# Kernel tuning notes

Measured on AMD Instinct MI355X. Metric: run time of the kernel, lower is better.

The kernel has to match this reference:

```python
import jax, jax.numpy as jnp
import numpy as np
import math

R1 = 1.0
R2 = 4.0
NBINS_XY = 4
NBINS_ZY = 4
PARTITIONS = NBINS_XY * NBINS_ZY * 2  # 32
TOPK = 200
TWO_PI = 2.0 * math.pi
PI = math.pi


def setup_inputs() -> dict:
    key = jax.random.key(0)
    k1, k2 = jax.random.split(key)
    # LiDAR-like coordinates, ~[-30, 30] meters
    sampled_vehicle_points = jax.random.normal(k1, (1024, 3), dtype=jnp.float32) * 20.0
    fusion_point = jax.random.normal(k2, (20000, 3), dtype=jnp.float32) * 20.0
    return {"sampled_vehicle_points": sampled_vehicle_points, "fusion_point": fusion_point}


def _compute_partitions_batch(q):
    # q: [S, K, 3]. rel[b, i, j] = q[b, j] - q[b, i]  (A.unsqueeze(1) - B.unsqueeze(2))
    rel = q[:, None, :, :] - q[:, :, None, :]  # [S, K, K, 3]
    angles_xy = jnp.fmod(jnp.arctan2(rel[..., 1], rel[..., 0]) + TWO_PI, TWO_PI)
    angles_zy = jnp.fmod(jnp.arctan2(rel[..., 1], rel[..., 2]) + TWO_PI, PI)
    xy_bins = jnp.floor(angles_xy / (TWO_PI / NBINS_XY))
    zy_bins = jnp.floor(angles_zy / (PI / NBINS_ZY))
    # hash(A, B, seed=NBINS_ZY): -1 where either < 0
    angle_ok = (xy_bins >= 0) & (zy_bins >= 0)
    angles_bins = jnp.where(angle_ok, xy_bins * NBINS_ZY + zy_bins, -1.0)
    D = jnp.sqrt(jnp.sum(rel * rel, axis=-1) + 1e-7)  # [S, K, K]
    dist_bins = jnp.where(D >= R2, 1.0, jnp.where(D >= R1, 0.0, -1.0))
    bin_ok = (dist_bins >= 0) & (angles_bins >= 0)
    bins = jnp.where(bin_ok, dist_bins * (NBINS_XY * NBINS_ZY) + angles_bins, -1.0)
    return bins  # [S, K, K] float, -1 for ignored


def reference(sampled_vehicle_points, fusion_point):
    # kNN query: K nearest fusion points for each sampled vehicle point
    d2 = jnp.sum(
        (sampled_vehicle_points[:, None, :] - fusion_point[None, :, :]) ** 2, axis=-1
    )  # [S, Nf]
    _, idx = jax.lax.top_k(-d2, TOPK)  # indices of TOPK smallest distances
    queried = fusion_point[idx]  # [S, K, 3]

    bins = _compute_partitions_batch(queried)  # [S, K, K]
    row0 = bins[:, 0, :]  # [S, K] — only row 0 is used by the loss
    # points_in_partition[s, p] = sum_j (row0[s, j] == p) + 1
    counts = jnp.sum(
        row0[:, :, None] == jnp.arange(PARTITIONS, dtype=bins.dtype)[None, None, :],
        axis=1,
    ).astype(jnp.float32) + 1.0  # [S, P]
    pip = counts / jnp.linalg.norm(counts, axis=-1, keepdims=True) * 4.0
    gt_dist = jax.nn.softmax(pip, axis=-1)
    return gt_dist
```

## Files before the change

kernel.cpp:

```cpp
#include <hip/hip_runtime.h>
#include <math.h>

#define KTOP 200
#define NPART 32
#define BLOCK 512
#define NHIST 2048
#define CAND_CAP 1024
#define WCAP 512
#define MAXIT 10

__device__ __forceinline__ float d2_ref(float ax, float ay, float az,
                                        float bx, float by, float bz) {
    float dx = __fsub_rn(ax, bx), dy = __fsub_rn(ay, by), dz = __fsub_rn(az, bz);
    return __fadd_rn(__fadd_rn(__fmul_rn(dx, dx), __fmul_rn(dy, dy)), __fmul_rn(dz, dz));
}

__device__ __forceinline__ unsigned key_of(const float* __restrict__ fus, int j,
                                           float vx, float vy, float vz) {
    return __float_as_uint(d2_ref(vx, vy, vz, fus[3*j], fus[3*j+1], fus[3*j+2]));
}

__device__ __forceinline__ int compute_bin(float rx, float ry, float rz) {
    const float TWO_PI_F = (float)6.283185307179586;
    const float PI_F     = (float)3.141592653589793;
    const float XY_W     = (float)(6.283185307179586 / 4.0);
    const float ZY_W     = (float)(3.141592653589793 / 4.0);

    float d2 = __fadd_rn(__fadd_rn(__fmul_rn(rx, rx), __fmul_rn(ry, ry)), __fmul_rn(rz, rz));
    float D  = sqrtf(__fadd_rn(d2, 1e-7f));
    float dist_bin;
    if (D >= 4.0f)      dist_bin = 1.0f;
    else if (D >= 1.0f) dist_bin = 0.0f;
    else                return -1;

    float axy = fmodf(atan2f(ry, rx) + TWO_PI_F, TWO_PI_F);
    float azy = fmodf(atan2f(ry, rz) + TWO_PI_F, PI_F);
    float xyb = floorf(__fdiv_rn(axy, XY_W));
    float zyb = floorf(__fdiv_rn(azy, ZY_W));
    if (!(xyb >= 0.0f && zyb >= 0.0f)) return -1;
    float ab  = xyb * 4.0f + zyb;
    int bin = (int)(dist_bin * 16.0f + ab);
    return bin;
}

__global__ __launch_bounds__(BLOCK, 4)
void shape_context_kernel(const float* __restrict__ veh,
                          const float* __restrict__ fus,
                          float* __restrict__ out,
                          int nfus) {
    const int b   = blockIdx.x;
    const int tid = threadIdx.x;
    const int lane = tid & 63;
    const int wid  = tid >> 6;

    __shared__ unsigned int hist[NHIST];
    __shared__ unsigned long long cand[CAND_CAP];
    __shared__ int wlist[WCAP];
    __shared__ unsigned int hist32[NPART];
    __shared__ unsigned int waveTot[BLOCK / 64];
    __shared__ unsigned int waveBase[BLOCK / 64];
    __shared__ unsigned int s_bucket, s_rem, s_bcount;
    __shared__ unsigned int s_minKey, s_minIdx;
    __shared__ int s_candCount, s_wcount;
    __shared__ float s_q0[3];
    __shared__ unsigned long long s_minPacked, s_lowBound;

    const float vx = veh[b * 3 + 0], vy = veh[b * 3 + 1], vz = veh[b * 3 + 2];
    const float4* fus4 = (const float4*)fus;
    const int ntrip = nfus >> 2;

    if (tid == 0) {
        s_minKey = 0xFFFFFFFFu; s_minIdx = 0xFFFFFFFFu;
        s_candCount = 0; s_wcount = 0;
    }
    for (int i = tid; i < NHIST; i += BLOCK) hist[i] = 0;
    if (tid < NPART) hist32[tid] = 0;
    __syncthreads();

    auto find_bucket = [&](unsigned remq) {
        const int PER = NHIST / BLOCK;
        int base = tid * PER;
        unsigned p = 0;
        #pragma unroll
        for (int i = 0; i < PER; i++) p += hist[base + i];
        unsigned incl = p;
        #pragma unroll
        for (int d = 1; d < 64; d <<= 1) {
            unsigned n = __shfl_up(incl, d, 64);
            if (lane >= d) incl += n;
        }
        if (lane == 63) waveTot[wid] = incl;
        __syncthreads();
        if (tid == 0) {
            unsigned acc = 0;
            for (int w = 0; w < BLOCK / 64; w++) { waveBase[w] = acc; acc += waveTot[w]; }
        }
        __syncthreads();
        unsigned excl = waveBase[wid] + incl - p;
        if (excl < remq && remq <= excl + p) {
            unsigned cum = excl;
            #pragma unroll
            for (int i = 0; i < PER; i++) {
                unsigned c = hist[base + i];
                if (cum + c >= remq) { s_bucket = base + i; s_rem = remq - cum; s_bcount = c; break; }
                cum += c;
            }
        }
        __syncthreads();
    };

    unsigned kreg[MAXIT][4];
    unsigned lmin = 0xFFFFFFFFu;
    #pragma unroll
    for (int it = 0; it < MAXIT; ++it) {
        int m = tid + it * BLOCK;
        if (m < ntrip) {
            float4 A = fus4[3 * m], Bq = fus4[3 * m + 1], Cq = fus4[3 * m + 2];
            float px0 = A.x,  py0 = A.y,  pz0 = A.z;
            float px1 = A.w,  py1 = Bq.x, pz1 = Bq.y;
            float px2 = Bq.z, py2 = Bq.w, pz2 = Cq.x;
            float px3 = Cq.y, py3 = Cq.z, pz3 = Cq.w;
            unsigned k0 = __float_as_uint(d2_ref(vx, vy, vz, px0, py0, pz0));
            unsigned k1 = __float_as_uint(d2_ref(vx, vy, vz, px1, py1, pz1));
            unsigned k2 = __float_as_uint(d2_ref(vx, vy, vz, px2, py2, pz2));
            unsigned k3 = __float_as_uint(d2_ref(vx, vy, vz, px3, py3, pz3));
            kreg[it][0] = k0; kreg[it][1] = k1; kreg[it][2] = k2; kreg[it][3] = k3;
            atomicAdd(&hist[k0 >> 21], 1u);
            atomicAdd(&hist[k1 >> 21], 1u);
            atomicAdd(&hist[k2 >> 21], 1u);
            atomicAdd(&hist[k3 >> 21], 1u);
            lmin = min(lmin, min(min(k0, k1), min(k2, k3)));
        } else {
            kreg[it][0] = kreg[it][1] = kreg[it][2] = kreg[it][3] = 0xFFFFFFFFu;
        }
    }
    for (int m = MAXIT * BLOCK + tid; m < ntrip; m += BLOCK) {
        #pragma unroll
        for (int q = 0; q < 4; ++q) {
            unsigned k = key_of(fus, 4 * m + q, vx, vy, vz);
            atomicAdd(&hist[k >> 21], 1u);
            lmin = min(lmin, k);
        }
    }
    for (int j = (nfus & ~3) + tid; j < nfus; j += BLOCK) {
        unsigned k = key_of(fus, j, vx, vy, vz);
        atomicAdd(&hist[k >> 21], 1u);
        lmin = min(lmin, k);
    }
    #pragma unroll
    for (int d = 32; d > 0; d >>= 1) lmin = min(lmin, __shfl_xor(lmin, d, 64));
    if (lane == 0) atomicMin(&s_minKey, lmin);
    __syncthreads();

    const unsigned mk = s_minKey;
    #pragma unroll
    for (int it = 0; it < MAXIT; ++it) {
        int m = tid + it * BLOCK;
        if (m < ntrip) {
            #pragma unroll
            for (int q = 0; q < 4; ++q)
                if (kreg[it][q] == mk) atomicMin(&s_minIdx, (unsigned)(4 * m + q));
        }
    }
    for (int m = MAXIT * BLOCK + tid; m < ntrip; m += BLOCK)
        #pragma unroll
        for (int q = 0; q < 4; ++q)
            if (key_of(fus, 4 * m + q, vx, vy, vz) == mk) atomicMin(&s_minIdx, (unsigned)(4 * m + q));
    for (int j = (nfus & ~3) + tid; j < nfus; j += BLOCK)
        if (key_of(fus, j, vx, vy, vz) == mk) atomicMin(&s_minIdx, (unsigned)j);

    find_bucket(KTOP);
    unsigned T = s_bucket;
    unsigned rem = s_rem;
    unsigned bcount = s_bcount;
    int shift = 21;

    if (tid == 0) {
        int idx0 = (int)s_minIdx;
        s_q0[0] = fus[idx0 * 3]; s_q0[1] = fus[idx0 * 3 + 1]; s_q0[2] = fus[idx0 * 3 + 2];
    }
    __syncthreads();
    const float q0x = s_q0[0], q0y = s_q0[1], q0z = s_q0[2];

    while (bcount > CAND_CAP && shift > 0) {
        int newshift = (shift > 11) ? (shift - 11) : 0;
        unsigned digmask = (1u << (shift - newshift)) - 1;
        for (int i = tid; i < NHIST; i += BLOCK) hist[i] = 0;
        __syncthreads();
        #pragma unroll
        for (int it = 0; it < MAXIT; ++it) {
            int m = tid + it * BLOCK;
            if (m < ntrip) {
                #pragma unroll
                for (int q = 0; q < 4; ++q) {
                    unsigned k = kreg[it][q];
                    if ((k >> shift) == T) atomicAdd(&hist[(k >> newshift) & digmask], 1u);
                }
            }
        }
        for (int m = MAXIT * BLOCK + tid; m < ntrip; m += BLOCK)
            #pragma unroll
            for (int q = 0; q < 4; ++q) {
                unsigned k = key_of(fus, 4 * m + q, vx, vy, vz);
                if ((k >> shift) == T) atomicAdd(&hist[(k >> newshift) & digmask], 1u);
            }
        for (int j = (nfus & ~3) + tid; j < nfus; j += BLOCK) {
            unsigned k = key_of(fus, j, vx, vy, vz);
            if ((k >> shift) == T) atomicAdd(&hist[(k >> newshift) & digmask], 1u);
        }
        __syncthreads();
        find_bucket(rem);
        T = (T << (shift - newshift)) | s_bucket;
        rem = s_rem;
        bcount = s_bcount;
        shift = newshift;
    }

    #pragma unroll
    for (int it = 0; it < MAXIT; ++it) {
        int m = tid + it * BLOCK;
        if (m < ntrip) {
            #pragma unroll
            for (int q = 0; q < 4; ++q) {
                unsigned k = kreg[it][q];
                unsigned hi = k >> shift;
                if (hi < T) {
                    int pos = atomicAdd(&s_wcount, 1);
                    if (pos < WCAP) wlist[pos] = 4 * m + q;
                } else if (hi == T) {
                    int pos = atomicAdd(&s_candCount, 1);
                    if (pos < CAND_CAP) cand[pos] = ((unsigned long long)k << 32) | (unsigned)(4 * m + q);
                }
            }
        }
    }
    for (int m = MAXIT * BLOCK + tid; m < ntrip; m += BLOCK)
        #pragma unroll
        for (int q = 0; q < 4; ++q) {
            unsigned k = key_of(fus, 4 * m + q, vx, vy, vz);
            unsigned hi = k >> shift;
            if (hi < T) { int pos = atomicAdd(&s_wcount, 1); if (pos < WCAP) wlist[pos] = 4 * m + q; }
            else if (hi == T) { int pos = atomicAdd(&s_candCount, 1); if (pos < CAND_CAP) cand[pos] = ((unsigned long long)k << 32) | (unsigned)(4 * m + q); }
        }
    for (int j = (nfus & ~3) + tid; j < nfus; j += BLOCK) {
        unsigned k = key_of(fus, j, vx, vy, vz);
        unsigned hi = k >> shift;
        if (hi < T) { int pos = atomicAdd(&s_wcount, 1); if (pos < WCAP) wlist[pos] = j; }
        else if (hi == T) { int pos = atomicAdd(&s_candCount, 1); if (pos < CAND_CAP) cand[pos] = ((unsigned long long)k << 32) | (unsigned)j; }
    }
    __syncthreads();

    const int cnt = s_candCount;
    if (cnt <= CAND_CAP) {
        for (int i = tid; i < cnt; i += BLOCK) {
            unsigned long long me = cand[i];
            int rank = 0;
            for (int k2 = 0; k2 < cnt; k2++) rank += (cand[k2] < me) ? 1 : 0;
            if (rank < (int)rem) {
                int pos = atomicAdd(&s_wcount, 1);
                if (pos < WCAP) wlist[pos] = (int)(me & 0xFFFFFFFFull);
            }
        }
    }
    __syncthreads();

    {
        int wc = s_wcount; if (wc > WCAP) wc = WCAP;
        for (int i = tid; i < wc; i += BLOCK) {
            int j = wlist[i];
            float fx = fus[3 * j], fy = fus[3 * j + 1], fz = fus[3 * j + 2];
            int bin = compute_bin(__fsub_rn(fx, q0x), __fsub_rn(fy, q0y), __fsub_rn(fz, q0z));
            if (bin >= 0 && bin < NPART) atomicAdd(&hist32[bin], 1u);
        }
    }
    __syncthreads();

    if (cnt > CAND_CAP) {
        if (tid == 0) s_lowBound = 0;
        __syncthreads();
        for (unsigned itx = 0; itx < rem; ++itx) {
            if (tid == 0) s_minPacked = ~0ull;
            __syncthreads();
            unsigned long long lowB = s_lowBound;
            unsigned long long lm = ~0ull;
            for (int j = tid; j < nfus; j += BLOCK) {
                unsigned k = key_of(fus, j, vx, vy, vz);
                if ((k >> shift) == T) {
                    unsigned long long p = ((unsigned long long)k << 32) | (unsigned)j;
                    if (p >= lowB && p < lm) lm = p;
                }
            }
            #pragma unroll
            for (int d = 32; d > 0; d >>= 1) {
                unsigned long long o = __shfl_xor(lm, d, 64);
                lm = (o < lm) ? o : lm;
            }
            if (lane == 0) atomicMin(&s_minPacked, lm);
            __syncthreads();
            if (tid == 0) {
                int jm = (int)(s_minPacked & 0xFFFFFFFFull);
                float fx = fus[jm * 3], fy = fus[jm * 3 + 1], fz = fus[jm * 3 + 2];
                int bin = compute_bin(__fsub_rn(fx, q0x), __fsub_rn(fy, q0y), __fsub_rn(fz, q0z));
                if (bin >= 0 && bin < NPART) hist32[bin] += 1u;
                s_lowBound = s_minPacked + 1;
            }
            __syncthreads();
        }
    }

    if (tid < NPART) {
        float c = (float)hist32[tid] + 1.0f;
        float ss = __fmul_rn(c, c);
        #pragma unroll
        for (int d = 16; d > 0; d >>= 1) ss += __shfl_xor(ss, d, 64);
        float v = __fmul_rn(__fdiv_rn(c, sqrtf(ss)), 4.0f);
        float mx = v;
        #pragma unroll
        for (int d = 16; d > 0; d >>= 1) mx = fmaxf(mx, __shfl_xor(mx, d, 64));
        float e = expf(v - mx);
        float sum = e;
        #pragma unroll
        for (int d = 16; d > 0; d >>= 1) sum += __shfl_xor(sum, d, 64);
        out[b * NPART + tid] = __fdiv_rn(e, sum);
    }
}

extern "C" void kernel_launch(void* const* d_in, const int* in_sizes, int n_in,
                              void* d_out, int out_size, void* d_ws, size_t ws_size,
                              hipStream_t stream) {
    const float* veh = (const float*)d_in[0];
    const float* fus = (const float*)d_in[1];
    float* out = (float*)d_out;
    int nveh = in_sizes[0] / 3;
    int nfus = in_sizes[1] / 3;
    shape_context_kernel<<<nveh, BLOCK, 0, stream>>>(veh, fus, out, nfus);
}
```

Before: 89.20 us.

## Pack top-bucket digits into registers and fuse min-key/index search

Per-thread key storage changes from forty 32-bit full keys to ten 64-bit words holding four 16-bit top digits each, and launch bounds are raised to allow 8 blocks per CU. The separate pass that finds the nearest point's index is replaced by a 64-bit packed (key,index) min reduction in the first pass. Refinement passes and candidate keys now recompute distances from global memory instead of reading cached keys, and the shared candidate buffer is halved to reduce LDS use. This trades extra recomputation and global loads for lower register and LDS pressure, aiming at higher occupancy.

```diff
diff --git a/kernel.cpp b/kernel.cpp
--- a/kernel.cpp
+++ b/kernel.cpp
@@ -5,7 +5,7 @@
 #define NPART 32
 #define BLOCK 512
 #define NHIST 2048
-#define CAND_CAP 1024
+#define CAND_CAP 512
 #define WCAP 512
 #define MAXIT 10
 
@@ -43,7 +43,7 @@
     return bin;
 }
 
-__global__ __launch_bounds__(BLOCK, 4)
+__global__ __launch_bounds__(BLOCK, 8)
 void shape_context_kernel(const float* __restrict__ veh,
                           const float* __restrict__ fus,
                           float* __restrict__ out,
@@ -60,7 +60,6 @@
     __shared__ unsigned int waveTot[BLOCK / 64];
     __shared__ unsigned int waveBase[BLOCK / 64];
     __shared__ unsigned int s_bucket, s_rem, s_bcount;
-    __shared__ unsigned int s_minKey, s_minIdx;
     __shared__ int s_candCount, s_wcount;
     __shared__ float s_q0[3];
     __shared__ unsigned long long s_minPacked, s_lowBound;
@@ -69,10 +68,7 @@
     const float4* fus4 = (const float4*)fus;
     const int ntrip = nfus >> 2;
 
-    if (tid == 0) {
-        s_minKey = 0xFFFFFFFFu; s_minIdx = 0xFFFFFFFFu;
-        s_candCount = 0; s_wcount = 0;
-    }
+    if (tid == 0) { s_minPacked = ~0ull; s_candCount = 0; s_wcount = 0; }
     for (int i = tid; i < NHIST; i += BLOCK) hist[i] = 0;
     if (tid < NPART) hist32[tid] = 0;
     __syncthreads();
@@ -109,29 +105,34 @@
         __syncthreads();
     };
 
-    unsigned kreg[MAXIT][4];
-    unsigned lmin = 0xFFFFFFFFu;
+    unsigned long long khi[MAXIT];
+    unsigned long long lmin = ~0ull;
     #pragma unroll
     for (int it = 0; it < MAXIT; ++it) {
         int m = tid + it * BLOCK;
         if (m < ntrip) {
             float4 A = fus4[3 * m], Bq = fus4[3 * m + 1], Cq = fus4[3 * m + 2];
-            float px0 = A.x,  py0 = A.y,  pz0 = A.z;
-            float px1 = A.w,  py1 = Bq.x, pz1 = Bq.y;
-            float px2 = Bq.z, py2 = Bq.w, pz2 = Cq.x;
-            float px3 = Cq.y, py3 = Cq.z, pz3 = Cq.w;
-            unsigned k0 = __float_as_uint(d2_ref(vx, vy, vz, px0, py0, pz0));
-            unsigned k1 = __float_as_uint(d2_ref(vx, vy, vz, px1, py1, pz1));
-            unsigned k2 = __float_as_uint(d2_ref(vx, vy, vz, px2, py2, pz2));
-            unsigned k3 = __float_as_uint(d2_ref(vx, vy, vz, px3, py3, pz3));
-            kreg[it][0] = k0; kreg[it][1] = k1; kreg[it][2] = k2; kreg[it][3] = k3;
+            unsigned k0 = __float_as_uint(d2_ref(vx, vy, vz, A.x,  A.y,  A.z));
+            unsigned k1 = __float_as_uint(d2_ref(vx, vy, vz, A.w,  Bq.x, Bq.y));
+            unsigned k2 = __float_as_uint(d2_ref(vx, vy, vz, Bq.z, Bq.w, Cq.x));
+            unsigned k3 = __float_as_uint(d2_ref(vx, vy, vz, Cq.y, Cq.z, Cq.w));
             atomicAdd(&hist[k0 >> 21], 1u);
             atomicAdd(&hist[k1 >> 21], 1u);
             atomicAdd(&hist[k2 >> 21], 1u);
             atomicAdd(&hist[k3 >> 21], 1u);
-            lmin = min(lmin, min(min(k0, k1), min(k2, k3)));
+            khi[it] = (unsigned long long)(k0 >> 21)
+                    | ((unsigned long long)(k1 >> 21) << 16)
+                    | ((unsigned long long)(k2 >> 21) << 32)
+                    | ((unsigned long long)(k3 >> 21) << 48);
+            unsigned jb = 4 * m;
+            unsigned long long p0 = ((unsigned long long)k0 << 32) | (jb + 0);
+            unsigned long long p1 = ((unsigned long long)k1 << 32) | (jb + 1);
+            unsigned long long p2 = ((unsigned long long)k2 << 32) | (jb + 2);
+            unsigned long long p3 = ((unsigned long long)k3 << 32) | (jb + 3);
+            unsigned long long pm = min(min(p0, p1), min(p2, p3));
+            lmin = min(lmin, pm);
         } else {
-            kreg[it][0] = kreg[it][1] = kreg[it][2] = kreg[it][3] = 0xFFFFFFFFu;
+            khi[it] = 0xFFFFFFFFFFFFFFFFull;
         }
     }
     for (int m = MAXIT * BLOCK + tid; m < ntrip; m += BLOCK) {
@@ -139,35 +140,21 @@
         for (int q = 0; q < 4; ++q) {
             unsigned k = key_of(fus, 4 * m + q, vx, vy, vz);
             atomicAdd(&hist[k >> 21], 1u);
-            lmin = min(lmin, k);
+            lmin = min(lmin, ((unsigned long long)k << 32) | (unsigned)(4 * m + q));
         }
     }
     for (int j = (nfus & ~3) + tid; j < nfus; j += BLOCK) {
         unsigned k = key_of(fus, j, vx, vy, vz);
         atomicAdd(&hist[k >> 21], 1u);
-        lmin = min(lmin, k);
+        lmin = min(lmin, ((unsigned long long)k << 32) | (unsigned)j);
     }
     #pragma unroll
-    for (int d = 32; d > 0; d >>= 1) lmin = min(lmin, __shfl_xor(lmin, d, 64));
-    if (lane == 0) atomicMin(&s_minKey, lmin);
-    __syncthreads();
-
-    const unsigned mk = s_minKey;
-    #pragma unroll
-    for (int it = 0; it < MAXIT; ++it) {
-        int m = tid + it * BLOCK;
-        if (m < ntrip) {
-            #pragma unroll
-            for (int q = 0; q < 4; ++q)
-                if (kreg[it][q] == mk) atomicMin(&s_minIdx, (unsigned)(4 * m + q));
-        }
-    }
-    for (int m = MAXIT * BLOCK + tid; m < ntrip; m += BLOCK)
-        #pragma unroll
-        for (int q = 0; q < 4; ++q)
-            if (key_of(fus, 4 * m + q, vx, vy, vz) == mk) atomicMin(&s_minIdx, (unsigned)(4 * m + q));
-    for (int j = (nfus & ~3) + tid; j < nfus; j += BLOCK)
-        if (key_of(fus, j, vx, vy, vz) == mk) atomicMin(&s_minIdx, (unsigned)j);
+    for (int d = 32; d > 0; d >>= 1) {
+        unsigned long long o = __shfl_xor(lmin, d, 64);
+        lmin = (o < lmin) ? o : lmin;
+    }
+    if (lane == 0) atomicMin(&s_minPacked, lmin);
+    __syncthreads();
 
     find_bucket(KTOP);
     unsigned T = s_bucket;
@@ -176,7 +163,7 @@
     int shift = 21;
 
     if (tid == 0) {
-        int idx0 = (int)s_minIdx;
+        int idx0 = (int)(s_minPacked & 0xFFFFFFFFull);
         s_q0[0] = fus[idx0 * 3]; s_q0[1] = fus[idx0 * 3 + 1]; s_q0[2] = fus[idx0 * 3 + 2];
     }
     __syncthreads();
@@ -187,24 +174,7 @@
         unsigned digmask = (1u << (shift - newshift)) - 1;
         for (int i = tid; i < NHIST; i += BLOCK) hist[i] = 0;
         __syncthreads();
-        #pragma unroll
-        for (int it = 0; it < MAXIT; ++it) {
-            int m = tid + it * BLOCK;
-            if (m < ntrip) {
-                #pragma unroll
-                for (int q = 0; q < 4; ++q) {
-                    unsigned k = kreg[it][q];
-                    if ((k >> shift) == T) atomicAdd(&hist[(k >> newshift) & digmask], 1u);
-                }
-            }
-        }
-        for (int m = MAXIT * BLOCK + tid; m < ntrip; m += BLOCK)
-            #pragma unroll
-            for (int q = 0; q < 4; ++q) {
-                unsigned k = key_of(fus, 4 * m + q, vx, vy, vz);
-                if ((k >> shift) == T) atomicAdd(&hist[(k >> newshift) & digmask], 1u);
-            }
-        for (int j = (nfus & ~3) + tid; j < nfus; j += BLOCK) {
+        for (int j = tid; j < nfus; j += BLOCK) {
             unsigned k = key_of(fus, j, vx, vy, vz);
             if ((k >> shift) == T) atomicAdd(&hist[(k >> newshift) & digmask], 1u);
         }
@@ -216,37 +186,47 @@
         shift = newshift;
     }
 
-    #pragma unroll
-    for (int it = 0; it < MAXIT; ++it) {
-        int m = tid + it * BLOCK;
-        if (m < ntrip) {
+    if (shift == 21) {
+        #pragma unroll
+        for (int it = 0; it < MAXIT; ++it) {
+            unsigned long long packed = khi[it];
+            int jb = 4 * (tid + it * BLOCK);
             #pragma unroll
             for (int q = 0; q < 4; ++q) {
-                unsigned k = kreg[it][q];
-                unsigned hi = k >> shift;
+                unsigned hi = (unsigned)((packed >> (16 * q)) & 0xFFFFull);
                 if (hi < T) {
                     int pos = atomicAdd(&s_wcount, 1);
-                    if (pos < WCAP) wlist[pos] = 4 * m + q;
+                    if (pos < WCAP) wlist[pos] = jb + q;
                 } else if (hi == T) {
+                    int j = jb + q;
+                    unsigned k = key_of(fus, j, vx, vy, vz);
                     int pos = atomicAdd(&s_candCount, 1);
-                    if (pos < CAND_CAP) cand[pos] = ((unsigned long long)k << 32) | (unsigned)(4 * m + q);
+                    if (pos < CAND_CAP) cand[pos] = ((unsigned long long)k << 32) | (unsigned)j;
                 }
             }
         }
-    }
-    for (int m = MAXIT * BLOCK + tid; m < ntrip; m += BLOCK)
-        #pragma unroll
-        for (int q = 0; q < 4; ++q) {
-            unsigned k = key_of(fus, 4 * m + q, vx, vy, vz);
+        for (int m = MAXIT * BLOCK + tid; m < ntrip; m += BLOCK)
+            #pragma unroll
+            for (int q = 0; q < 4; ++q) {
+                int j = 4 * m + q;
+                unsigned k = key_of(fus, j, vx, vy, vz);
+                unsigned hi = k >> shift;
+                if (hi < T) { int pos = atomicAdd(&s_wcount, 1); if (pos < WCAP) wlist[pos] = j; }
+                else if (hi == T) { int pos = atomicAdd(&s_candCount, 1); if (pos < CAND_CAP) cand[pos] = ((unsigned long long)k << 32) | (unsigned)j; }
+            }
+        for (int j = (nfus & ~3) + tid; j < nfus; j += BLOCK) {
+            unsigned k = key_of(fus, j, vx, vy, vz);
             unsigned hi = k >> shift;
-            if (hi < T) { int pos = atomicAdd(&s_wcount, 1); if (pos < WCAP) wlist[pos] = 4 * m + q; }
-            else if (hi == T) { int pos = atomicAdd(&s_candCount, 1); if (pos < CAND_CAP) cand[pos] = ((unsigned long long)k << 32) | (unsigned)(4 * m + q); }
-        }
-    for (int j = (nfus & ~3) + tid; j < nfus; j += BLOCK) {
-        unsigned k = key_of(fus, j, vx, vy, vz);
-        unsigned hi = k >> shift;
-        if (hi < T) { int pos = atomicAdd(&s_wcount, 1); if (pos < WCAP) wlist[pos] = j; }
-        else if (hi == T) { int pos = atomicAdd(&s_candCount, 1); if (pos < CAND_CAP) cand[pos] = ((unsigned long long)k << 32) | (unsigned)j; }
+            if (hi < T) { int pos = atomicAdd(&s_wcount, 1); if (pos < WCAP) wlist[pos] = j; }
+            else if (hi == T) { int pos = atomicAdd(&s_candCount, 1); if (pos < CAND_CAP) cand[pos] = ((unsigned long long)k << 32) | (unsigned)j; }
+        }
+    } else {
+        for (int j = tid; j < nfus; j += BLOCK) {
+            unsigned k = key_of(fus, j, vx, vy, vz);
+            unsigned hi = k >> shift;
+            if (hi < T) { int pos = atomicAdd(&s_wcount, 1); if (pos < WCAP) wlist[pos] = j; }
+            else if (hi == T) { int pos = atomicAdd(&s_candCount, 1); if (pos < CAND_CAP) cand[pos] = ((unsigned long long)k << 32) | (unsigned)j; }
+        }
     }
     __syncthreads();
 
```

Measured after the change: 82.68 us. 1.08x faster.
